# Kernel optimization log

Measured on AMD Instinct MI355X. Metric: run time of the kernel, lower is better.

## Reference

```python
import jax, jax.numpy as jnp
import numpy as np

B, G, N, C = 8, 16, 1024, 256


def setup_inputs() -> dict:
    key = jax.random.key(0)
    k1, k2, k3, k4, k5 = jax.random.split(key, 5)
    x = jax.random.normal(k1, (B, G, N, C), dtype=jnp.float32)
    vs = jax.random.normal(k2, (B, G, 1, N, 3), dtype=jnp.float32)
    s = 1.0 / np.sqrt(C)
    W_fc = jax.random.normal(k3, (C, C), dtype=jnp.float32) * s   # nn.Linear weight [out,in]
    b_fc = jax.random.normal(k4, (C,), dtype=jnp.float32) * s
    W_vn = jax.random.normal(k5, (C, C), dtype=jnp.float32) * s   # VNLinear weight [out,in], no bias
    return {"x": x, "vs": vs, "W_fc": W_fc, "b_fc": b_fc, "W_vn": W_vn}


def reference(x, vs, W_fc, b_fc, W_vn):
    # q = fc(x): [B,G,N,C]
    q = jnp.einsum('bgnc,oc->bgno', x, W_fc) + b_fc
    # softmax over the point dim N (torch dim=2)
    atten = jax.nn.softmax(q, axis=2)
    xw = atten * x  # [B,G,N,C]
    # torch: expand to [B,G,C,N,3] * vs then sum over N.
    # Equivalent contraction without materializing the 5D tensor:
    v = jnp.squeeze(vs, axis=2)  # [B,G,N,3]
    out = jnp.einsum('bgnc,bgnd->bgcd', xw, v)  # [B,G,C,3]
    # VNLinear: bias-free linear over channel dim, shared across the 3 vector comps
    return jnp.einsum('bgcd,oc->bgod', out, W_vn)  # [B,G,C,3]
```

## Files before the change

### kernel.cpp

```cpp
#include <hip/hip_runtime.h>
#include <hip/hip_bf16.h>


#define NQ 1024
#define CQ 256
#define CT 64
#define RT 128
#define NT (NQ / RT)
#define XS 136

typedef __attribute__((ext_vector_type(8))) short bf16x8;
typedef __attribute__((ext_vector_type(4))) float f32x4;

__device__ __forceinline__ ushort2 pk2(float a, float b) {
    __hip_bfloat162 h = __float22bfloat162_rn(make_float2(a, b));
    ushort2 r;
    __builtin_memcpy(&r, &h, sizeof(r));
    return r;
}
__device__ __forceinline__ float bf2f(ushort h) {
    union { unsigned u; float f; } v; v.u = ((unsigned)h) << 16;
    return v.f;
}

__global__ __launch_bounds__(256, 2)
void fused_attn_pool_mfma(const float* __restrict__ x, const float* __restrict__ vs,
                          const float* __restrict__ Wfc, const float* __restrict__ Wvn,
                          float* __restrict__ out) {
    __shared__ __align__(16) ushort xs[RT * XS];
    __shared__ __align__(16) float  vsm[RT * 3];
    __shared__ f32x4 red[4][32];
    __shared__ float Tsm[CT][3];

    const int t = threadIdx.x;
    const int id = blockIdx.x;
    const int ctile = (id >> 3) & 3;
    const int bg = (id & 7) + ((id >> 5) << 3);
    const int c0 = ctile * CT;
    const int own = ctile >> 1;

    const int w = t >> 6, lane = t & 63;
    const int quad = lane >> 4, l16 = lane & 15;
    const int rstrip = (w & 1) * 64;
    const int cstrip = (w >> 1) * 32;

    const float* xb = x + (size_t)bg * NQ * CQ;
    const float* vb = vs + (size_t)bg * NQ * 3;

    bf16x8 bf[2][4][2];
    {
        const int myc0 = c0 + cstrip + l16;
        #pragma unroll
        for (int kc = 0; kc < 2; ++kc) {
            const int ch = (kc == 0) ? (own ^ 1) : own;
            const int kb = ch * 128 + quad * 8;
            #pragma unroll
            for (int ks = 0; ks < 4; ++ks) {
                #pragma unroll
                for (int ci = 0; ci < 2; ++ci) {
                    const float* p = Wfc + (size_t)(myc0 + ci * 16) * CQ + kb + ks * 32;
                    float4 lo = *reinterpret_cast<const float4*>(p);
                    float4 hi = *reinterpret_cast<const float4*>(p + 4);
                    ushort2 p0 = pk2(lo.x, lo.y), p1 = pk2(lo.z, lo.w);
                    ushort2 p2 = pk2(hi.x, hi.y), p3 = pk2(hi.z, hi.w);
                    bf[kc][ks][ci] = (bf16x8){ (short)p0.x, (short)p0.y, (short)p1.x, (short)p1.y,
                                               (short)p2.x, (short)p2.y, (short)p3.x, (short)p3.y };
                }
            }
        }
    }

    float rZ[2] = {0.f, 0.f}, rS0[2] = {0.f, 0.f}, rS1[2] = {0.f, 0.f}, rS2[2] = {0.f, 0.f};

    for (int nt = 0; nt < NT; ++nt) {
        const int n0 = nt * RT;
        if (t < 96) {
            reinterpret_cast<float4*>(vsm)[t] =
                reinterpret_cast<const float4*>(vb + (size_t)n0 * 3)[t];
        }

        f32x4 acc[4][2];
        #pragma unroll
        for (int m = 0; m < 4; ++m)
            #pragma unroll
            for (int ci = 0; ci < 2; ++ci) acc[m][ci] = (f32x4){0.f, 0.f, 0.f, 0.f};

        #pragma unroll
        for (int kc = 0; kc < 2; ++kc) {
            const int ch = (kc == 0) ? (own ^ 1) : own;
            const int kc0 = ch * 128;
            #pragma unroll
            for (int p = 0; p < 16; ++p) {
                int idx = p * 256 + t;
                int row = idx >> 5, k4 = idx & 31;
                float4 v4 = *reinterpret_cast<const float4*>(
                    xb + (size_t)(n0 + row) * CQ + kc0 + k4 * 4);
                ushort2 a0 = pk2(v4.x, v4.y), a1 = pk2(v4.z, v4.w);
                ushort4 pk = { a0.x, a0.y, a1.x, a1.y };
                *reinterpret_cast<ushort4*>(&xs[row * XS + k4 * 4]) = pk;
            }
            __syncthreads();
            #pragma unroll
            for (int ks = 0; ks < 4; ++ks) {
                const int kk = ks * 32 + quad * 8;
                #pragma unroll
                for (int m = 0; m < 4; ++m) {
                    bf16x8 a = *reinterpret_cast<const bf16x8*>(
                        &xs[(rstrip + m * 16 + l16) * XS + kk]);
                    acc[m][0] = __builtin_amdgcn_mfma_f32_16x16x32_bf16(a, bf[kc][ks][0], acc[m][0], 0, 0, 0);
                    acc[m][1] = __builtin_amdgcn_mfma_f32_16x16x32_bf16(a, bf[kc][ks][1], acc[m][1], 0, 0, 0);
                }
            }
            if (kc == 0) __syncthreads();
        }
        const int xcb = (ctile & 1) * 64 + cstrip;

        #pragma unroll
        for (int m = 0; m < 4; ++m) {
            const int rbase = rstrip + m * 16 + quad * 4;
            float v0[4], v1[4], v2[4];
            #pragma unroll
            for (int r = 0; r < 4; ++r) {
                v0[r] = vsm[(rbase + r) * 3 + 0];
                v1[r] = vsm[(rbase + r) * 3 + 1];
                v2[r] = vsm[(rbase + r) * 3 + 2];
            }
            #pragma unroll
            for (int ci = 0; ci < 2; ++ci) {
                const int xc = xcb + ci * 16 + l16;
                #pragma unroll
                for (int r = 0; r < 4; ++r) {
                    float e = __expf(acc[m][ci][r]);
                    float xv = bf2f(xs[(rbase + r) * XS + xc]);
                    rZ[ci] += e;
                    float p = e * xv;
                    rS0[ci] = fmaf(p, v0[r], rS0[ci]);
                    rS1[ci] = fmaf(p, v1[r], rS1[ci]);
                    rS2[ci] = fmaf(p, v2[r], rS2[ci]);
                }
            }
        }
        __syncthreads();
    }

    #pragma unroll
    for (int ci = 0; ci < 2; ++ci) {
        float z = rZ[ci], s0 = rS0[ci], s1 = rS1[ci], s2 = rS2[ci];
        #pragma unroll
        for (int off = 16; off < 64; off <<= 1) {
            z  += __shfl_xor(z,  off);
            s0 += __shfl_xor(s0, off);
            s1 += __shfl_xor(s1, off);
            s2 += __shfl_xor(s2, off);
        }
        if (quad == 0) red[w][ci * 16 + l16] = (f32x4){z, s0, s1, s2};
    }
    __syncthreads();
    if (t < CT) {
        const int s = t >> 5, cc = t & 31;
        f32x4 a = red[2 * s][cc], b = red[2 * s + 1][cc];
        float inv = 1.f / (a[0] + b[0]);
        Tsm[t][0] = (a[1] + b[1]) * inv;
        Tsm[t][1] = (a[2] + b[2]) * inv;
        Tsm[t][2] = (a[3] + b[3]) * inv;
    }
    __syncthreads();

    {
        const float* wr = Wvn + (size_t)t * CQ + c0;
        float a0 = 0.f, a1 = 0.f, a2 = 0.f;
        #pragma unroll
        for (int c = 0; c < CT; c += 4) {
            float4 w4 = *reinterpret_cast<const float4*>(wr + c);
            a0 += w4.x * Tsm[c + 0][0] + w4.y * Tsm[c + 1][0]
                + w4.z * Tsm[c + 2][0] + w4.w * Tsm[c + 3][0];
            a1 += w4.x * Tsm[c + 0][1] + w4.y * Tsm[c + 1][1]
                + w4.z * Tsm[c + 2][1] + w4.w * Tsm[c + 3][1];
            a2 += w4.x * Tsm[c + 0][2] + w4.y * Tsm[c + 1][2]
                + w4.z * Tsm[c + 2][2] + w4.w * Tsm[c + 3][2];
        }
        float* op = out + ((size_t)bg * CQ + t) * 3;
        atomicAdd(&op[0], a0);
        atomicAdd(&op[1], a1);
        atomicAdd(&op[2], a2);
    }
}

extern "C" void kernel_launch(void* const* d_in, const int* in_sizes, int n_in,
                              void* d_out, int out_size, void* d_ws, size_t ws_size,
                              hipStream_t stream) {
    const float* x   = (const float*)d_in[0];
    const float* vs  = (const float*)d_in[1];
    const float* Wfc = (const float*)d_in[2];
    const float* Wvn = (const float*)d_in[4];
    float* out = (float*)d_out;

    (void)hipMemsetAsync(out, 0, (size_t)out_size * sizeof(float), stream);
    fused_attn_pool_mfma<<<dim3(512), dim3(256), 0, stream>>>(x, vs, Wfc, Wvn, out);
}
```

Before: 221.6 us.

## Split point dimension across blocks and move VN projection to separate kernel

The main kernel now splits the N=1024 point dimension into two halves, doubling the grid to 1024 blocks. Each block atomically accumulates unnormalized softmax sums (Z, S0..S2) into a workspace buffer. A second small kernel normalizes those sums and applies the VN linear with wave-level shuffle reductions. The goal is more parallelism and occupancy, with launch_bounds raised to 4 blocks per CU. This costs an extra kernel launch, extra atomics and a workspace round trip.

```diff
diff --git a/kernel.cpp b/kernel.cpp
--- a/kernel.cpp
+++ b/kernel.cpp
@@ -6,7 +6,7 @@
 #define CQ 256
 #define CT 64
 #define RT 128
-#define NT (NQ / RT)
+#define NTB 4
 #define XS 136
 
 typedef __attribute__((ext_vector_type(8))) short bf16x8;
@@ -23,19 +23,19 @@
     return v.f;
 }
 
-__global__ __launch_bounds__(256, 2)
+__global__ __launch_bounds__(256, 4)
 void fused_attn_pool_mfma(const float* __restrict__ x, const float* __restrict__ vs,
-                          const float* __restrict__ Wfc, const float* __restrict__ Wvn,
-                          float* __restrict__ out) {
+                          const float* __restrict__ Wfc, float* __restrict__ wsacc) {
     __shared__ __align__(16) ushort xs[RT * XS];
     __shared__ __align__(16) float  vsm[RT * 3];
     __shared__ f32x4 red[4][32];
-    __shared__ float Tsm[CT][3];
 
     const int t = threadIdx.x;
     const int id = blockIdx.x;
-    const int ctile = (id >> 3) & 3;
-    const int bg = (id & 7) + ((id >> 5) << 3);
+    const int sub = (id >> 3) & 7;
+    const int bg = (id & 7) + ((id >> 6) << 3);
+    const int ctile = sub & 3;
+    const int nh = sub >> 2;
     const int c0 = ctile * CT;
     const int own = ctile >> 1;
 
@@ -72,8 +72,8 @@
 
     float rZ[2] = {0.f, 0.f}, rS0[2] = {0.f, 0.f}, rS1[2] = {0.f, 0.f}, rS2[2] = {0.f, 0.f};
 
-    for (int nt = 0; nt < NT; ++nt) {
-        const int n0 = nt * RT;
+    for (int nt = 0; nt < NTB; ++nt) {
+        const int n0 = nh * (NTB * RT) + nt * RT;
         if (t < 96) {
             reinterpret_cast<float4*>(vsm)[t] =
                 reinterpret_cast<const float4*>(vb + (size_t)n0 * 3)[t];
@@ -159,30 +159,48 @@
     if (t < CT) {
         const int s = t >> 5, cc = t & 31;
         f32x4 a = red[2 * s][cc], b = red[2 * s + 1][cc];
-        float inv = 1.f / (a[0] + b[0]);
-        Tsm[t][0] = (a[1] + b[1]) * inv;
-        Tsm[t][1] = (a[2] + b[2]) * inv;
-        Tsm[t][2] = (a[3] + b[3]) * inv;
+        float* p = wsacc + ((size_t)bg * CQ + c0 + t) * 4;
+        atomicAdd(p + 0, a[0] + b[0]);
+        atomicAdd(p + 1, a[1] + b[1]);
+        atomicAdd(p + 2, a[2] + b[2]);
+        atomicAdd(p + 3, a[3] + b[3]);
+    }
+}
+
+__global__ __launch_bounds__(256)
+void vn_norm(const float* __restrict__ wsacc, const float* __restrict__ Wvn,
+             float* __restrict__ out) {
+    __shared__ __align__(16) float Ts[CQ][3];
+    const int bg = blockIdx.x >> 1, half = blockIdx.x & 1;
+    const int t = threadIdx.x, wv = t >> 6, lane = t & 63;
+    {
+        float4 a = reinterpret_cast<const float4*>(wsacc)[(size_t)bg * CQ + t];
+        float inv = 1.f / a.x;
+        Ts[t][0] = a.y * inv; Ts[t][1] = a.z * inv; Ts[t][2] = a.w * inv;
     }
     __syncthreads();
-
-    {
-        const float* wr = Wvn + (size_t)t * CQ + c0;
-        float a0 = 0.f, a1 = 0.f, a2 = 0.f;
-        #pragma unroll
-        for (int c = 0; c < CT; c += 4) {
-            float4 w4 = *reinterpret_cast<const float4*>(wr + c);
-            a0 += w4.x * Tsm[c + 0][0] + w4.y * Tsm[c + 1][0]
-                + w4.z * Tsm[c + 2][0] + w4.w * Tsm[c + 3][0];
-            a1 += w4.x * Tsm[c + 0][1] + w4.y * Tsm[c + 1][1]
-                + w4.z * Tsm[c + 2][1] + w4.w * Tsm[c + 3][1];
-            a2 += w4.x * Tsm[c + 0][2] + w4.y * Tsm[c + 1][2]
-                + w4.z * Tsm[c + 2][2] + w4.w * Tsm[c + 3][2];
-        }
-        float* op = out + ((size_t)bg * CQ + t) * 3;
-        atomicAdd(&op[0], a0);
-        atomicAdd(&op[1], a1);
-        atomicAdd(&op[2], a2);
+    const int c = lane * 4;
+    float t00 = Ts[c+0][0], t01 = Ts[c+0][1], t02 = Ts[c+0][2];
+    float t10 = Ts[c+1][0], t11 = Ts[c+1][1], t12 = Ts[c+1][2];
+    float t20 = Ts[c+2][0], t21 = Ts[c+2][1], t22 = Ts[c+2][2];
+    float t30 = Ts[c+3][0], t31 = Ts[c+3][1], t32 = Ts[c+3][2];
+    const int obase = half * 128 + wv * 32;
+    for (int i = 0; i < 32; ++i) {
+        const int o = obase + i;
+        float4 w4 = *reinterpret_cast<const float4*>(Wvn + (size_t)o * CQ + c);
+        float a0 = w4.x*t00 + w4.y*t10 + w4.z*t20 + w4.w*t30;
+        float a1 = w4.x*t01 + w4.y*t11 + w4.z*t21 + w4.w*t31;
+        float a2 = w4.x*t02 + w4.y*t12 + w4.z*t22 + w4.w*t32;
+        #pragma unroll
+        for (int off = 1; off < 64; off <<= 1) {
+            a0 += __shfl_xor(a0, off);
+            a1 += __shfl_xor(a1, off);
+            a2 += __shfl_xor(a2, off);
+        }
+        if (lane == 0) {
+            float* op = out + ((size_t)bg * CQ + o) * 3;
+            op[0] = a0; op[1] = a1; op[2] = a2;
+        }
     }
 }
 
@@ -194,7 +212,9 @@
     const float* Wfc = (const float*)d_in[2];
     const float* Wvn = (const float*)d_in[4];
     float* out = (float*)d_out;
-
-    (void)hipMemsetAsync(out, 0, (size_t)out_size * sizeof(float), stream);
-    fused_attn_pool_mfma<<<dim3(512), dim3(256), 0, stream>>>(x, vs, Wfc, Wvn, out);
-}
+    float* wsacc = (float*)d_ws;
+
+    (void)hipMemsetAsync(wsacc, 0, (size_t)128 * CQ * 4 * sizeof(float), stream);
+    fused_attn_pool_mfma<<<dim3(1024), dim3(256), 0, stream>>>(x, vs, Wfc, wsacc);
+    vn_norm<<<dim3(256), dim3(256), 0, stream>>>(wsacc, Wvn, out);
+}
```

Result: slower. 373.1 us (+68.3%).

## Split sequence dimension across blocks with atomic partial softmax accumulation

Applied to the files above, without the earlier changes.

Splits the N dimension into four chunks so the grid grows from 512 to 2048 blocks, each processing 64-row tiles. Partial softmax sums and weighted sums go to a workspace through atomics, and the last arriving block (found via a counter) finishes the normalisation and the VNLinear projection. A prep kernel zeroes the workspace and output and pre-converts Wfc to bf16, so B fragments are loaded from global per k-step instead of being held in registers. The aim is more parallelism and lower register pressure, at the cost of extra atomics, a second launch and repeated weight loads.

```diff
diff --git a/kernel.cpp b/kernel.cpp
--- a/kernel.cpp
+++ b/kernel.cpp
@@ -5,8 +5,9 @@
 #define NQ 1024
 #define CQ 256
 #define CT 64
-#define RT 128
-#define NT (NQ / RT)
+#define RT 64
+#define NTB 4
+#define NH 4
 #define XS 136
 
 typedef __attribute__((ext_vector_type(8))) short bf16x8;
@@ -23,65 +24,67 @@
     return v.f;
 }
 
+#define WSACC_F4   32768
+#define CNT_OFF    (512 * 1024)
+#define WFB_OFF    (CNT_OFF + 2048)
+
+__global__ __launch_bounds__(256)
+void prep(const float* __restrict__ Wfc, ushort* __restrict__ wfb,
+          float* __restrict__ wsacc, unsigned* __restrict__ cnt,
+          float* __restrict__ out) {
+    const int tid = blockIdx.x * 256 + threadIdx.x;
+    reinterpret_cast<float4*>(wsacc)[tid] = (float4){0.f, 0.f, 0.f, 0.f};
+    if (tid < 512) cnt[tid] = 0u;
+    if (tid < 24576) reinterpret_cast<float4*>(out)[tid] = (float4){0.f, 0.f, 0.f, 0.f};
+    if (tid < 16384) {
+        float4 v = reinterpret_cast<const float4*>(Wfc)[tid];
+        ushort2 a = pk2(v.x, v.y), b = pk2(v.z, v.w);
+        ushort4 pk = { a.x, a.y, b.x, b.y };
+        reinterpret_cast<ushort4*>(wfb)[tid] = pk;
+    }
+}
+
 __global__ __launch_bounds__(256, 2)
 void fused_attn_pool_mfma(const float* __restrict__ x, const float* __restrict__ vs,
-                          const float* __restrict__ Wfc, const float* __restrict__ Wvn,
+                          const ushort* __restrict__ wfb, float* __restrict__ wsacc,
+                          unsigned* __restrict__ cnt, const float* __restrict__ Wvn,
                           float* __restrict__ out) {
     __shared__ __align__(16) ushort xs[RT * XS];
     __shared__ __align__(16) float  vsm[RT * 3];
     __shared__ f32x4 red[4][32];
     __shared__ float Tsm[CT][3];
+    __shared__ int flag;
 
     const int t = threadIdx.x;
     const int id = blockIdx.x;
-    const int ctile = (id >> 3) & 3;
-    const int bg = (id & 7) + ((id >> 5) << 3);
+    const int sub = (id >> 3) & 15;
+    const int bg = (id & 7) + ((id >> 7) << 3);
+    const int ctile = sub & 3;
+    const int nh = sub >> 2;
     const int c0 = ctile * CT;
     const int own = ctile >> 1;
 
     const int w = t >> 6, lane = t & 63;
     const int quad = lane >> 4, l16 = lane & 15;
-    const int rstrip = (w & 1) * 64;
+    const int rstrip = (w & 1) * 32;
     const int cstrip = (w >> 1) * 32;
+    const int myc0 = c0 + cstrip + l16;
 
     const float* xb = x + (size_t)bg * NQ * CQ;
     const float* vb = vs + (size_t)bg * NQ * 3;
 
-    bf16x8 bf[2][4][2];
-    {
-        const int myc0 = c0 + cstrip + l16;
-        #pragma unroll
-        for (int kc = 0; kc < 2; ++kc) {
-            const int ch = (kc == 0) ? (own ^ 1) : own;
-            const int kb = ch * 128 + quad * 8;
-            #pragma unroll
-            for (int ks = 0; ks < 4; ++ks) {
-                #pragma unroll
-                for (int ci = 0; ci < 2; ++ci) {
-                    const float* p = Wfc + (size_t)(myc0 + ci * 16) * CQ + kb + ks * 32;
-                    float4 lo = *reinterpret_cast<const float4*>(p);
-                    float4 hi = *reinterpret_cast<const float4*>(p + 4);
-                    ushort2 p0 = pk2(lo.x, lo.y), p1 = pk2(lo.z, lo.w);
-                    ushort2 p2 = pk2(hi.x, hi.y), p3 = pk2(hi.z, hi.w);
-                    bf[kc][ks][ci] = (bf16x8){ (short)p0.x, (short)p0.y, (short)p1.x, (short)p1.y,
-                                               (short)p2.x, (short)p2.y, (short)p3.x, (short)p3.y };
-                }
-            }
-        }
-    }
-
     float rZ[2] = {0.f, 0.f}, rS0[2] = {0.f, 0.f}, rS1[2] = {0.f, 0.f}, rS2[2] = {0.f, 0.f};
 
-    for (int nt = 0; nt < NT; ++nt) {
-        const int n0 = nt * RT;
-        if (t < 96) {
+    for (int nt = 0; nt < NTB; ++nt) {
+        const int n0 = nh * (NTB * RT) + nt * RT;
+        if (t < 48) {
             reinterpret_cast<float4*>(vsm)[t] =
                 reinterpret_cast<const float4*>(vb + (size_t)n0 * 3)[t];
         }
 
-        f32x4 acc[4][2];
-        #pragma unroll
-        for (int m = 0; m < 4; ++m)
+        f32x4 acc[2][2];
+        #pragma unroll
+        for (int m = 0; m < 2; ++m)
             #pragma unroll
             for (int ci = 0; ci < 2; ++ci) acc[m][ci] = (f32x4){0.f, 0.f, 0.f, 0.f};
 
@@ -90,7 +93,7 @@
             const int ch = (kc == 0) ? (own ^ 1) : own;
             const int kc0 = ch * 128;
             #pragma unroll
-            for (int p = 0; p < 16; ++p) {
+            for (int p = 0; p < 8; ++p) {
                 int idx = p * 256 + t;
                 int row = idx >> 5, k4 = idx & 31;
                 float4 v4 = *reinterpret_cast<const float4*>(
@@ -103,12 +106,14 @@
             #pragma unroll
             for (int ks = 0; ks < 4; ++ks) {
                 const int kk = ks * 32 + quad * 8;
+                bf16x8 b0 = *reinterpret_cast<const bf16x8*>(&wfb[(size_t)myc0 * CQ + kc0 + kk]);
+                bf16x8 b1 = *reinterpret_cast<const bf16x8*>(&wfb[(size_t)(myc0 + 16) * CQ + kc0 + kk]);
                 #pragma unroll
-                for (int m = 0; m < 4; ++m) {
+                for (int m = 0; m < 2; ++m) {
                     bf16x8 a = *reinterpret_cast<const bf16x8*>(
                         &xs[(rstrip + m * 16 + l16) * XS + kk]);
-                    acc[m][0] = __builtin_amdgcn_mfma_f32_16x16x32_bf16(a, bf[kc][ks][0], acc[m][0], 0, 0, 0);
-                    acc[m][1] = __builtin_amdgcn_mfma_f32_16x16x32_bf16(a, bf[kc][ks][1], acc[m][1], 0, 0, 0);
+                    acc[m][0] = __builtin_amdgcn_mfma_f32_16x16x32_bf16(a, b0, acc[m][0], 0, 0, 0);
+                    acc[m][1] = __builtin_amdgcn_mfma_f32_16x16x32_bf16(a, b1, acc[m][1], 0, 0, 0);
                 }
             }
             if (kc == 0) __syncthreads();
@@ -116,7 +121,7 @@
         const int xcb = (ctile & 1) * 64 + cstrip;
 
         #pragma unroll
-        for (int m = 0; m < 4; ++m) {
+        for (int m = 0; m < 2; ++m) {
             const int rbase = rstrip + m * 16 + quad * 4;
             float v0[4], v1[4], v2[4];
             #pragma unroll
@@ -159,13 +164,31 @@
     if (t < CT) {
         const int s = t >> 5, cc = t & 31;
         f32x4 a = red[2 * s][cc], b = red[2 * s + 1][cc];
-        float inv = 1.f / (a[0] + b[0]);
-        Tsm[t][0] = (a[1] + b[1]) * inv;
-        Tsm[t][1] = (a[2] + b[2]) * inv;
-        Tsm[t][2] = (a[3] + b[3]) * inv;
-    }
-    __syncthreads();
-
+        float* p = wsacc + ((size_t)bg * CQ + c0 + t) * 4;
+        atomicAdd(p + 0, a[0] + b[0]);
+        atomicAdd(p + 1, a[1] + b[1]);
+        atomicAdd(p + 2, a[2] + b[2]);
+        atomicAdd(p + 3, a[3] + b[3]);
+    }
+    __syncthreads();
+    if (t == 0) {
+        __threadfence();
+        flag = (int)atomicAdd(&cnt[bg * 4 + ctile], 1u);
+    }
+    __syncthreads();
+    if (flag != NH - 1) return;
+
+    if (t < CT) {
+        __threadfence();
+        const float* p = wsacc + ((size_t)bg * CQ + c0 + t) * 4;
+        float Z  = __hip_atomic_load(p + 0, __ATOMIC_RELAXED, __HIP_MEMORY_SCOPE_AGENT);
+        float S0 = __hip_atomic_load(p + 1, __ATOMIC_RELAXED, __HIP_MEMORY_SCOPE_AGENT);
+        float S1 = __hip_atomic_load(p + 2, __ATOMIC_RELAXED, __HIP_MEMORY_SCOPE_AGENT);
+        float S2 = __hip_atomic_load(p + 3, __ATOMIC_RELAXED, __HIP_MEMORY_SCOPE_AGENT);
+        float inv = 1.f / Z;
+        Tsm[t][0] = S0 * inv; Tsm[t][1] = S1 * inv; Tsm[t][2] = S2 * inv;
+    }
+    __syncthreads();
     {
         const float* wr = Wvn + (size_t)t * CQ + c0;
         float a0 = 0.f, a1 = 0.f, a2 = 0.f;
@@ -195,6 +218,11 @@
     const float* Wvn = (const float*)d_in[4];
     float* out = (float*)d_out;
 
-    (void)hipMemsetAsync(out, 0, (size_t)out_size * sizeof(float), stream);
-    fused_attn_pool_mfma<<<dim3(512), dim3(256), 0, stream>>>(x, vs, Wfc, Wvn, out);
-}
+    char* ws = (char*)d_ws;
+    float*    wsacc = (float*)ws;
+    unsigned* cnt   = (unsigned*)(ws + CNT_OFF);
+    ushort*   wfb   = (ushort*)(ws + WFB_OFF);
+
+    prep<<<dim3(128), dim3(256), 0, stream>>>(Wfc, wfb, wsacc, cnt, out);
+    fused_attn_pool_mfma<<<dim3(2048), dim3(256), 0, stream>>>(x, vs, wfb, wsacc, cnt, Wvn, out);
+}
```

Result: slower. 373.8 us (+68.7%).
